# Kernel tuning notes

Measured on AMD Instinct MI355X. Metric: run time of the kernel, lower is better.

The kernel has to match this reference:

```python
import jax, jax.numpy as jnp
import numpy as np

T, B, D, H = 1024, 64, 512, 512


def setup_inputs() -> dict:
    key = jax.random.key(0)
    ks = jax.random.split(key, 10)
    s_in = 1.0 / np.sqrt(D + H)  # torch Linear default init scale
    inp = {
        "inputs": jax.random.normal(ks[0], (T, B, D), dtype=jnp.float32),
        "Wf": jax.random.uniform(ks[1], (D + H, H), jnp.float32, -s_in, s_in),
        "bf": jax.random.uniform(ks[2], (H,), jnp.float32, -s_in, s_in),
        "Wi": jax.random.uniform(ks[3], (D + H, H), jnp.float32, -s_in, s_in),
        "bi": jax.random.uniform(ks[4], (H,), jnp.float32, -s_in, s_in),
        "Wg": jax.random.uniform(ks[5], (D + H, H), jnp.float32, -s_in, s_in),
        "bg": jax.random.uniform(ks[6], (H,), jnp.float32, -s_in, s_in),
        "Wo": jax.random.uniform(ks[7], (D + H, H), jnp.float32, -s_in, s_in),
        "bo": jax.random.uniform(ks[8], (H,), jnp.float32, -s_in, s_in),
        "phase_bias": jax.random.normal(ks[9], (H,), dtype=jnp.float32) * 0.02,
    }
    return inp


def reference(inputs, Wf, bf, Wi, bi, Wg, bg, Wo, bo, phase_bias):
    gate_scale = 1.0
    Bsz = inputs.shape[1]
    Hd = Wf.shape[1]
    # Fuse the four gate projections into one GEMM per step (same math).
    W = jnp.concatenate([Wf, Wi, Wg, Wo], axis=1)          # [D+H, 4H]
    bias = jnp.concatenate([bf, bi, bg, bo]) * gate_scale + jnp.tile(phase_bias, 4)
    # note: (x@W + b)*s + pb == x@(W*s) + (b*s + pb); gate_scale folded in.
    Ws = W * gate_scale

    h0 = jnp.zeros((Bsz, Hd), dtype=inputs.dtype)
    c0 = jnp.zeros((Bsz, Hd), dtype=inputs.dtype)

    def step(carry, x):
        hx, cx = carry
        combined = jnp.concatenate([x, hx], axis=1)         # [B, D+H]
        z = combined @ Ws + bias                            # [B, 4H]
        zf, zi, zg, zo = jnp.split(z, 4, axis=1)
        f = jax.nn.sigmoid(zf)
        i = jax.nn.sigmoid(zi)
        g = jnp.tanh(zg)
        o = jax.nn.sigmoid(zo)
        cx = f * cx + i * g
        hx = o * jnp.tanh(cx)
        return (hx, cx), hx

    (hx, cx), stacked = jax.lax.scan(step, (h0, c0), inputs)
    return stacked, hx, cx
```

## Files before the change

### kernel.cpp

```cpp
#include <hip/hip_runtime.h>

#define TT 1024
#define BB 64
#define DD 512
#define HH 512
#define NG 4
#define BPG 16
#define NS 32
#define NTHR 256

typedef short s8v __attribute__((ext_vector_type(8)));
typedef float f4v __attribute__((ext_vector_type(4)));
typedef int i4v __attribute__((ext_vector_type(4)));

static __device__ __forceinline__ unsigned short f2bf(float f) {
  union { float f; unsigned int u; } v; v.f = f;
  unsigned int r = v.u + 0x7FFFu + ((v.u >> 16) & 1u);
  return (unsigned short)(r >> 16);
}
static __device__ __forceinline__ i4v ld_b128_cohere(const void* p) {
  i4v r;
  asm volatile("global_load_dwordx4 %0, %1, off sc0 sc1"
               : "=v"(r) : "v"(p) : "memory");
  return r;
}
static __device__ __forceinline__ int ld_b32_cohere(const void* p) {
  int r;
  asm volatile("global_load_dword %0, %1, off sc0 sc1\n\t"
               "s_waitcnt vmcnt(0)"
               : "=v"(r) : "v"(p) : "memory");
  return r;
}
static __device__ __forceinline__ void st_b32_cohere(void* p, unsigned int v) {
  asm volatile("global_store_dword %0, %1, off sc0 sc1"
               :: "v"(p), "v"(v) : "memory");
}
static __device__ __forceinline__ unsigned int cvtpk_bf16(float lo, float hi) {
  unsigned int r;
  asm("v_cvt_pk_bf16_f32 %0, %1, %2" : "=v"(r) : "v"(lo), "v"(hi));
  return r;
}

__global__ void __launch_bounds__(128, 1) qlstm_init(int* flags) {
  st_b32_cohere(flags + threadIdx.x, 0u);
}

__global__ void __launch_bounds__(NTHR, 1) qlstm_main(
    const float* __restrict__ X,
    const float* __restrict__ Wf, const float* __restrict__ bfp,
    const float* __restrict__ Wi, const float* __restrict__ bip,
    const float* __restrict__ Wg, const float* __restrict__ bgp,
    const float* __restrict__ Wo, const float* __restrict__ bop,
    const float* __restrict__ phase,
    float* __restrict__ out, int* __restrict__ flags,
    unsigned short* __restrict__ hbuf) {
  __shared__ float zx[2][2][4][64][4];
  __shared__ float zh[2][4][64][4];
  const int tid   = threadIdx.x;
  const int wv    = tid >> 6;
  const int lane  = tid & 63;
  const int n     = lane & 15;
  const int kg    = lane >> 4;
  const int group = blockIdx.x & (NG - 1);
  const int slice = blockIdx.x >> 2;
  const int b0 = group * BPG;
  const int u0 = slice * 16;
  const bool isH = (wv >= 2);
  const int kh = wv & 1;

  const int wcol = u0 + (n & 7);
  s8v wreg[4][8];
#pragma unroll
  for (int T = 0; T < 4; ++T) {
    const float* Wsel = (T & 1) ? ((n < 8) ? Wg : Wo) : ((n < 8) ? Wf : Wi);
    const float* Wp = Wsel + (size_t)((isH ? 512 : 0) + kh * 256 + kg * 8) * HH
                    + wcol + (T >> 1) * 8;
#pragma unroll
    for (int kc = 0; kc < 8; ++kc)
#pragma unroll
      for (int j = 0; j < 8; ++j)
        wreg[T][kc][j] = (short)f2bf(Wp[(size_t)(kc * 32 + j) * HH]);
  }

  const int gb = tid >> 4, gu = tid & 15;
  const int uu = u0 + gu;
  const float bzf = bfp[uu] + phase[uu];
  const float bzi = bip[uu] + phase[uu];
  const float bzg = bgp[uu] + phase[uu];
  const float bzo = bop[uu] + phase[uu];
  float cst = 0.f;

  for (int p = tid; p < 2 * 4 * 64 * 4; p += NTHR) ((float*)zh)[p] = 0.f;
  float4 xv[16];
  s8v xf[8];
  if (!isH) {
    const float* Xr = X + ((size_t)0 * BB + b0 + n) * DD + kh * 256 + kg * 8;
#pragma unroll
    for (int kc = 0; kc < 8; ++kc) {
      xv[2 * kc]     = *(const float4*)(Xr + kc * 32);
      xv[2 * kc + 1] = *(const float4*)(Xr + kc * 32 + 4);
    }
#pragma unroll
    for (int kc = 0; kc < 8; ++kc) {
      union { s8v s; unsigned int d[4]; } af;
      af.d[0] = cvtpk_bf16(xv[2 * kc].x, xv[2 * kc].y);
      af.d[1] = cvtpk_bf16(xv[2 * kc].z, xv[2 * kc].w);
      af.d[2] = cvtpk_bf16(xv[2 * kc + 1].x, xv[2 * kc + 1].y);
      af.d[3] = cvtpk_bf16(xv[2 * kc + 1].z, xv[2 * kc + 1].w);
      xf[kc] = af.s;
    }
    f4v acc[4] = {{0.f,0.f,0.f,0.f},{0.f,0.f,0.f,0.f},{0.f,0.f,0.f,0.f},{0.f,0.f,0.f,0.f}};
#pragma unroll
    for (int kc = 0; kc < 8; ++kc)
#pragma unroll
      for (int T = 0; T < 4; ++T)
        acc[T] = __builtin_amdgcn_mfma_f32_16x16x32_bf16(xf[kc], wreg[T][kc], acc[T], 0, 0, 0);
#pragma unroll
    for (int T = 0; T < 4; ++T) *(f4v*)&zx[0][kh][T][lane][0] = acc[T];
    const float* X1 = X + ((size_t)1 * BB + b0 + n) * DD + kh * 256 + kg * 8;
#pragma unroll
    for (int kc = 0; kc < 8; ++kc) {
      xv[2 * kc]     = *(const float4*)(X1 + kc * 32);
      xv[2 * kc + 1] = *(const float4*)(X1 + kc * 32 + 4);
    }
  }

  int* myflag = flags + group * NS + slice;
  const int* pollp = flags + group * NS + (lane & 31);

  for (int t = 0; t < TT; ++t) {
    if (!isH) {
      if (t + 1 < TT) {
#pragma unroll
        for (int kc = 0; kc < 8; ++kc) {
          union { s8v s; unsigned int d[4]; } af;
          af.d[0] = cvtpk_bf16(xv[2 * kc].x, xv[2 * kc].y);
          af.d[1] = cvtpk_bf16(xv[2 * kc].z, xv[2 * kc].w);
          af.d[2] = cvtpk_bf16(xv[2 * kc + 1].x, xv[2 * kc + 1].y);
          af.d[3] = cvtpk_bf16(xv[2 * kc + 1].z, xv[2 * kc + 1].w);
          xf[kc] = af.s;
        }
        f4v acc[4] = {{0.f,0.f,0.f,0.f},{0.f,0.f,0.f,0.f},{0.f,0.f,0.f,0.f},{0.f,0.f,0.f,0.f}};
#pragma unroll
        for (int kc = 0; kc < 8; ++kc)
#pragma unroll
          for (int T = 0; T < 4; ++T)
            acc[T] = __builtin_amdgcn_mfma_f32_16x16x32_bf16(xf[kc], wreg[T][kc], acc[T], 0, 0, 0);
#pragma unroll
        for (int T = 0; T < 4; ++T)
          *(f4v*)&zx[(t + 1) & 1][kh][T][lane][0] = acc[T];
      }
    } else if (t > 0) {
      for (;;) {
        const int v = ld_b32_cohere(pollp);
        if (__all(v >= t)) break;
        __builtin_amdgcn_s_sleep(1);
      }
      const unsigned short* hb = hbuf + (size_t)((t - 1) & 1) * BB * HH +
                                 (size_t)(b0 + n) * HH + kh * 256 + kg * 8;
      i4v hf[8];
#pragma unroll
      for (int kc = 0; kc < 8; ++kc) hf[kc] = ld_b128_cohere(hb + kc * 32);
      asm volatile("s_waitcnt vmcnt(0)" ::: "memory");
      __builtin_amdgcn_sched_barrier(0);
      f4v acc[4] = {{0.f,0.f,0.f,0.f},{0.f,0.f,0.f,0.f},{0.f,0.f,0.f,0.f},{0.f,0.f,0.f,0.f}};
#pragma unroll
      for (int kc = 0; kc < 8; ++kc) {
        union { i4v i; s8v s; } af; af.i = hf[kc];
#pragma unroll
        for (int T = 0; T < 4; ++T)
          acc[T] = __builtin_amdgcn_mfma_f32_16x16x32_bf16(af.s, wreg[T][kc], acc[T], 0, 0, 0);
      }
#pragma unroll
      for (int T = 0; T < 4; ++T) *(f4v*)&zh[kh][T][lane][0] = acc[T];
    }
    __syncthreads();

    const int par = t & 1;
    const int Lf  = (gb >> 2) * 16 + (gu & 7);
    const int T0  = (gu >> 3) * 2;
    const int ci  = gb & 3;
    const float zfv = zx[par][0][T0][Lf][ci]     + zx[par][1][T0][Lf][ci]
                    + zh[0][T0][Lf][ci]          + zh[1][T0][Lf][ci] + bzf;
    const float ziv = zx[par][0][T0][Lf+8][ci]   + zx[par][1][T0][Lf+8][ci]
                    + zh[0][T0][Lf+8][ci]        + zh[1][T0][Lf+8][ci] + bzi;
    const float zgv = zx[par][0][T0+1][Lf][ci]   + zx[par][1][T0+1][Lf][ci]
                    + zh[0][T0+1][Lf][ci]        + zh[1][T0+1][Lf][ci] + bzg;
    const float zov = zx[par][0][T0+1][Lf+8][ci] + zx[par][1][T0+1][Lf+8][ci]
                    + zh[0][T0+1][Lf+8][ci]      + zh[1][T0+1][Lf+8][ci] + bzo;
    const float fg = 1.f / (1.f + __expf(-zfv));
    const float ig = 1.f / (1.f + __expf(-ziv));
    const float gg = 1.f - 2.f / (__expf(2.f * zgv) + 1.f);
    const float og = 1.f / (1.f + __expf(-zov));
    cst = fg * cst + ig * gg;
    const float hv = og * (1.f - 2.f / (__expf(2.f * cst) + 1.f));

    const float hn = __shfl_down(hv, 1);
    if (!(gu & 1))
      st_b32_cohere(hbuf + (size_t)par * BB * HH + (size_t)(b0 + gb) * HH + uu,
                    cvtpk_bf16(hv, hn));
    asm volatile("s_waitcnt vmcnt(0)" ::: "memory");
    if (!isH && t + 2 < TT) {
      const float* Xr = X + ((size_t)(t + 2) * BB + b0 + n) * DD + kh * 256 + kg * 8;
#pragma unroll
      for (int kc = 0; kc < 8; ++kc) {
        xv[2 * kc]     = *(const float4*)(Xr + kc * 32);
        xv[2 * kc + 1] = *(const float4*)(Xr + kc * 32 + 4);
      }
    }
    __syncthreads();
    if (tid == 0) st_b32_cohere(myflag, (unsigned int)(t + 1));

    out[(size_t)t * BB * HH + (size_t)(b0 + gb) * HH + uu] = hv;
    if (t == TT - 1) {
      out[(size_t)TT * BB * HH + (size_t)(b0 + gb) * HH + uu] = hv;
      out[(size_t)TT * BB * HH + BB * HH + (size_t)(b0 + gb) * HH + uu] = cst;
    }
  }
}

extern "C" void kernel_launch(void* const* d_in, const int* in_sizes, int n_in,
                              void* d_out, int out_size, void* d_ws,
                              size_t ws_size, hipStream_t stream) {
  const float* X   = (const float*)d_in[0];
  const float* Wf  = (const float*)d_in[1];
  const float* bfp = (const float*)d_in[2];
  const float* Wi  = (const float*)d_in[3];
  const float* bip = (const float*)d_in[4];
  const float* Wg  = (const float*)d_in[5];
  const float* bgp = (const float*)d_in[6];
  const float* Wo  = (const float*)d_in[7];
  const float* bop = (const float*)d_in[8];
  const float* ph  = (const float*)d_in[9];
  float* out = (float*)d_out;

  int* flags = (int*)d_ws;
  unsigned short* hbuf = (unsigned short*)((char*)d_ws + 4096);

  qlstm_init<<<1, 128, 0, stream>>>(flags);
  qlstm_main<<<NG * NS, NTHR, 0, stream>>>(X, Wf, bfp, Wi, bip, Wg, bgp, Wo,
                                           bop, ph, out, flags, hbuf);
}
```

Measured before the change: 3.121 ms.

## Tag hidden-state words with step index to replace flag polling

Each packed bf16 pair of the hidden state is now stored with the step index in a 64-bit word. Consumers load h speculatively and validate the tags, so they skip the separate flag poll whenever the data is already present, and fall back to polling only on a mismatch. The pre-store wait and barrier are also moved so that the X prefetch and output writes come before the end-of-step barrier. The cost is twice the h traffic and extra register pressure (16 vector loads). Ordering is weaker because the producer's flag is still written before the h stores are confirmed, and validity now relies on the tag check.

```diff
diff --git a/kernel.cpp b/kernel.cpp
--- a/kernel.cpp
+++ b/kernel.cpp
@@ -35,6 +35,11 @@
   asm volatile("global_store_dword %0, %1, off sc0 sc1"
                :: "v"(p), "v"(v) : "memory");
 }
+static __device__ __forceinline__ void st_b64_cohere(void* p,
+                                                     unsigned long long v) {
+  asm volatile("global_store_dwordx2 %0, %1, off sc0 sc1"
+               :: "v"(p), "v"(v) : "memory");
+}
 static __device__ __forceinline__ unsigned int cvtpk_bf16(float lo, float hi) {
   unsigned int r;
   asm("v_cvt_pk_bf16_f32 %0, %1, %2" : "=v"(r) : "v"(lo), "v"(hi));
@@ -53,7 +58,7 @@
     const float* __restrict__ Wo, const float* __restrict__ bop,
     const float* __restrict__ phase,
     float* __restrict__ out, int* __restrict__ flags,
-    unsigned short* __restrict__ hbuf) {
+    unsigned long long* __restrict__ hbuf64) {
   __shared__ float zx[2][2][4][64][4];
   __shared__ float zh[2][4][64][4];
   const int tid   = threadIdx.x;
@@ -151,22 +156,41 @@
           *(f4v*)&zx[(t + 1) & 1][kh][T][lane][0] = acc[T];
       }
     } else if (t > 0) {
-      for (;;) {
-        const int v = ld_b32_cohere(pollp);
-        if (__all(v >= t)) break;
-        __builtin_amdgcn_s_sleep(1);
-      }
-      const unsigned short* hb = hbuf + (size_t)((t - 1) & 1) * BB * HH +
-                                 (size_t)(b0 + n) * HH + kh * 256 + kg * 8;
-      i4v hf[8];
-#pragma unroll
-      for (int kc = 0; kc < 8; ++kc) hf[kc] = ld_b128_cohere(hb + kc * 32);
-      asm volatile("s_waitcnt vmcnt(0)" ::: "memory");
-      __builtin_amdgcn_sched_barrier(0);
+      const int tm1 = t - 1;
+      const unsigned long long* hb = hbuf64 + (size_t)(tm1 & 1) * BB * 256 +
+                                     (size_t)(b0 + n) * 256 + kh * 128 + kg * 4;
+      i4v hf[16];
+      for (int attempt = 0; ; ++attempt) {
+#pragma unroll
+        for (int kc = 0; kc < 8; ++kc) {
+          hf[2 * kc]     = ld_b128_cohere(hb + kc * 16);
+          hf[2 * kc + 1] = ld_b128_cohere(hb + kc * 16 + 2);
+        }
+        asm volatile("s_waitcnt vmcnt(0)" ::: "memory");
+        __builtin_amdgcn_sched_barrier(0);
+        int bad = 0;
+#pragma unroll
+        for (int j = 0; j < 16; ++j)
+          bad |= (hf[j][1] ^ tm1) | (hf[j][3] ^ tm1);
+        if (__all(bad == 0)) break;
+        if (attempt == 0) {
+          for (;;) {
+            const int v = ld_b32_cohere(pollp);
+            if (__all(v >= t)) break;
+            __builtin_amdgcn_s_sleep(1);
+          }
+        } else {
+          __builtin_amdgcn_s_sleep(1);
+        }
+      }
       f4v acc[4] = {{0.f,0.f,0.f,0.f},{0.f,0.f,0.f,0.f},{0.f,0.f,0.f,0.f},{0.f,0.f,0.f,0.f}};
 #pragma unroll
       for (int kc = 0; kc < 8; ++kc) {
-        union { i4v i; s8v s; } af; af.i = hf[kc];
+        union { i4v i; s8v s; } af;
+        af.i[0] = hf[2 * kc][0];
+        af.i[1] = hf[2 * kc][2];
+        af.i[2] = hf[2 * kc + 1][0];
+        af.i[3] = hf[2 * kc + 1][2];
 #pragma unroll
         for (int T = 0; T < 4; ++T)
           acc[T] = __builtin_amdgcn_mfma_f32_16x16x32_bf16(af.s, wreg[T][kc], acc[T], 0, 0, 0);
@@ -196,19 +220,13 @@
     const float hv = og * (1.f - 2.f / (__expf(2.f * cst) + 1.f));
 
     const float hn = __shfl_down(hv, 1);
-    if (!(gu & 1))
-      st_b32_cohere(hbuf + (size_t)par * BB * HH + (size_t)(b0 + gb) * HH + uu,
-                    cvtpk_bf16(hv, hn));
-    asm volatile("s_waitcnt vmcnt(0)" ::: "memory");
-    if (!isH && t + 2 < TT) {
-      const float* Xr = X + ((size_t)(t + 2) * BB + b0 + n) * DD + kh * 256 + kg * 8;
-#pragma unroll
-      for (int kc = 0; kc < 8; ++kc) {
-        xv[2 * kc]     = *(const float4*)(Xr + kc * 32);
-        xv[2 * kc + 1] = *(const float4*)(Xr + kc * 32 + 4);
-      }
-    }
-    __syncthreads();
+    if (!(gu & 1)) {
+      const unsigned long long d =
+          ((unsigned long long)(unsigned)t << 32) |
+          (unsigned long long)cvtpk_bf16(hv, hn);
+      st_b64_cohere(hbuf64 + (size_t)par * BB * 256 +
+                        (size_t)(b0 + gb) * 256 + (uu >> 1), d);
+    }
     if (tid == 0) st_b32_cohere(myflag, (unsigned int)(t + 1));
 
     out[(size_t)t * BB * HH + (size_t)(b0 + gb) * HH + uu] = hv;
@@ -216,6 +234,15 @@
       out[(size_t)TT * BB * HH + (size_t)(b0 + gb) * HH + uu] = hv;
       out[(size_t)TT * BB * HH + BB * HH + (size_t)(b0 + gb) * HH + uu] = cst;
     }
+    if (!isH && t + 2 < TT) {
+      const float* Xr = X + ((size_t)(t + 2) * BB + b0 + n) * DD + kh * 256 + kg * 8;
+#pragma unroll
+      for (int kc = 0; kc < 8; ++kc) {
+        xv[2 * kc]     = *(const float4*)(Xr + kc * 32);
+        xv[2 * kc + 1] = *(const float4*)(Xr + kc * 32 + 4);
+      }
+    }
+    __syncthreads();
   }
 }
 
@@ -235,9 +262,9 @@
   float* out = (float*)d_out;
 
   int* flags = (int*)d_ws;
-  unsigned short* hbuf = (unsigned short*)((char*)d_ws + 4096);
+  unsigned long long* hbuf64 = (unsigned long long*)((char*)d_ws + 4096);
 
   qlstm_init<<<1, 128, 0, stream>>>(flags);
   qlstm_main<<<NG * NS, NTHR, 0, stream>>>(X, Wf, bfp, Wi, bip, Wg, bgp, Wo,
-                                           bop, ph, out, flags, hbuf);
-}
+                                           bop, ph, out, flags, hbuf64);
+}
```

New measurement: 3.879 ms. +24.3%, slower.
